# Performance work log

Hardware: AMD Instinct MI355X
Metric: run time of the kernel (lower is better)

## Reference

```python
import jax, jax.numpy as jnp
import numpy as np

N_NODES = 50000
N_EDGES = 800000
IN_CH = 64
OUT_CH = 64
HEADS = 4
NEG_SLOPE = 0.2  # PyG GATConv default


def setup_inputs() -> dict:
    key = jax.random.key(0)
    ks = jax.random.split(key, 8)
    x = jax.random.normal(ks[0], (N_NODES, IN_CH), dtype=jnp.float32)
    edge_index = jax.random.randint(ks[1], (2, N_EDGES), 0, N_NODES, dtype=jnp.int64)
    # GATConv params (concat=False): lin weight [in, H*out], att vectors [H, out], bias [out]
    W = jax.random.normal(ks[2], (IN_CH, HEADS * OUT_CH), dtype=jnp.float32) * (1.0 / np.sqrt(IN_CH))
    att_src = jax.random.normal(ks[3], (HEADS, OUT_CH), dtype=jnp.float32) * 0.1
    att_dst = jax.random.normal(ks[4], (HEADS, OUT_CH), dtype=jnp.float32) * 0.1
    bias = jnp.zeros((OUT_CH,), dtype=jnp.float32)
    fc_w = jax.random.normal(ks[5], (OUT_CH, 1), dtype=jnp.float32) * (1.0 / np.sqrt(OUT_CH))
    fc_b = jnp.zeros((1,), dtype=jnp.float32)
    return {"x": x, "edge_index": edge_index, "W": W, "att_src": att_src,
            "att_dst": att_dst, "bias": bias, "fc_w": fc_w, "fc_b": fc_b}


def reference(x, edge_index, W, att_src, att_dst, bias, fc_w, fc_b):
    N = x.shape[0]
    H, C = att_src.shape
    # per-node linear transform -> [N, H, C]
    xt = (x @ W).reshape(N, H, C)
    # PyG default add_self_loops=True
    loop = jnp.arange(N, dtype=edge_index.dtype)
    src = jnp.concatenate([edge_index[0], loop])  # message source j
    dst = jnp.concatenate([edge_index[1], loop])  # aggregation target i
    # attention logits: a_l . x_j + a_r . x_i, leaky_relu
    a_src = jnp.einsum('nhc,hc->nh', xt, att_src)  # [N, H]
    a_dst = jnp.einsum('nhc,hc->nh', xt, att_dst)
    e = jax.nn.leaky_relu(a_src[src] + a_dst[dst], NEG_SLOPE)  # [E, H]
    # segment softmax over incoming edges of each dst node
    m = jax.ops.segment_max(e, dst, num_segments=N)            # [N, H]
    e = jnp.exp(e - m[dst])
    s = jax.ops.segment_sum(e, dst, num_segments=N)            # [N, H]
    alpha = e / s[dst]                                          # [E, H]
    # weighted scatter-aggregate
    msg = xt[src] * alpha[:, :, None]                           # [E, H, C]
    out = jax.ops.segment_sum(msg, dst, num_segments=N)         # [N, H, C]
    out = out.mean(axis=1) + bias                               # concat=False -> mean heads
    h = jax.nn.relu(out)
    scores = (h @ fc_w + fc_b).squeeze(-1)                      # [N]
    return scores
```

## Files before the change

kernel.cpp:

```cpp
#include <hip/hip_runtime.h>
#include <hip/hip_bf16.h>

#define N_NODES 50000
#define N_EDGES 800000
#define HEADS   4
#define NEG_SLOPE 0.2f
#define CAP     64
#define NT      ((N_NODES + 63) / 64)
#define EPB     2048
#define NREG    391
#define NREP    8
#define QSUB    384
#define NAGG    (N_NODES / 16)
#define INV_LN2 1.44269504088896340736f

typedef __attribute__((ext_vector_type(8))) _Float16 half8;
typedef __attribute__((ext_vector_type(4))) float f32x4;
typedef __attribute__((ext_vector_type(8))) unsigned short u16x8;

template <typename T> __device__ __forceinline__ float cvt(T v);
template <> __device__ __forceinline__ float cvt<float>(float v) { return v; }
template <> __device__ __forceinline__ float cvt<__hip_bfloat16>(__hip_bfloat16 v) {
    return __bfloat162float(v);
}
__device__ __forceinline__ unsigned short f2h(float f) {
    _Float16 h = (_Float16)f;
    return __builtin_bit_cast(unsigned short, h);
}
__device__ __forceinline__ float hbits(unsigned short u) {
    return (float)__builtin_bit_cast(_Float16, u);
}
__device__ __forceinline__ int probe_fp32(const unsigned* xw) {
    int sane = 0;
    for (int j = 0; j < 64; ++j) {
        unsigned e = (xw[j] >> 7) & 0xFF;
        sane += (e >= 90 && e <= 141);
    }
    return sane < 32;
}
__device__ __forceinline__ float loadW(int isf32, const void* W, int idx) {
    return isf32 ? ((const float*)W)[idx]
                 : cvt<__hip_bfloat16>(((const __hip_bfloat16*)W)[idx]);
}

template <typename T>
__device__ __forceinline__ void load8_f16(const T* p, _Float16* dst);
template <>
__device__ __forceinline__ void load8_f16<float>(const float* p, _Float16* dst) {
    float4 a = *(const float4*)p;
    float4 b = *(const float4*)(p + 4);
    dst[0] = (_Float16)a.x; dst[1] = (_Float16)a.y;
    dst[2] = (_Float16)a.z; dst[3] = (_Float16)a.w;
    dst[4] = (_Float16)b.x; dst[5] = (_Float16)b.y;
    dst[6] = (_Float16)b.z; dst[7] = (_Float16)b.w;
}
template <>
__device__ __forceinline__ void load8_f16<__hip_bfloat16>(const __hip_bfloat16* p,
                                                          _Float16* dst) {
    uint4 a = *(const uint4*)p;
    const unsigned short* u = (const unsigned short*)&a;
#pragma unroll
    for (int j = 0; j < 8; ++j)
        dst[j] = (_Float16)__uint_as_float(((unsigned)u[j]) << 16);
}

__global__ __launch_bounds__(256) void k_init(const unsigned* __restrict__ xw,
                                              const int* __restrict__ ei,
                                              const void* __restrict__ W,
                                              const void* __restrict__ att_src,
                                              const void* __restrict__ att_dst,
                                              int* __restrict__ qcnt,
                                              int* __restrict__ flags,
                                              unsigned short* __restrict__ Batt,
                                              unsigned short* __restrict__ Bpost) {
    __shared__ float waS[256], waD[256];
    __shared__ int f32sh;
    if (blockIdx.x == 0) {
        for (int t = threadIdx.x; t < NREP * NREG; t += 256) qcnt[t] = 0;
        if (threadIdx.x == 0) {
            int all0 = 1;
            for (int j = 1; j < 64; j += 2) all0 &= (ei[j] == 0);
            flags[0] = all0;
            flags[1] = probe_fp32(xw);
        }
        return;
    }
    const int pb = blockIdx.x - 1;
    if (threadIdx.x == 0) f32sh = probe_fp32(xw);
    __syncthreads();
    const int isf32 = f32sh;
    if (pb == 0) {
        int t = threadIdx.x, k = t >> 2, h = t & 3;
        float s = 0.f, d = 0.f;
        for (int c = 0; c < 64; ++c) {
            float w = loadW(isf32, W, k * 256 + h * 64 + c);
            float as = isf32 ? ((const float*)att_src)[h * 64 + c]
                             : cvt<__hip_bfloat16>(((const __hip_bfloat16*)att_src)[h * 64 + c]);
            float ad = isf32 ? ((const float*)att_dst)[h * 64 + c]
                             : cvt<__hip_bfloat16>(((const __hip_bfloat16*)att_dst)[h * 64 + c]);
            s = fmaf(w, as, s);
            d = fmaf(w, ad, d);
        }
        waS[t] = s * INV_LN2;
        waD[t] = d * INV_LN2;
        __syncthreads();
        if (threadIdx.x < 128) {
            int r = threadIdx.x;
            int q = (r >> 6) & 1, l = r & 63, n = l & 15;
            int kbase = q * 32 + ((l >> 4) & 3) * 8;
#pragma unroll
            for (int j = 0; j < 8; ++j) {
                int kk = kbase + j;
                float v = (n < 4) ? waS[kk * 4 + n]
                        : (n < 8) ? waD[kk * 4 + (n - 4)] : 0.f;
                Batt[r * 8 + j] = f2h(v);
            }
        }
    } else {
        const int sub = threadIdx.x >> 5, s = threadIdx.x & 31;
        const int t = (pb - 1) * 8 + sub;
        const int kt = t >> 2, nt = t & 3;
#pragma unroll
        for (int e = 0; e < 16; ++e) {
            int idx = s * 16 + e;
            int l = idx >> 3, j = idx & 7;
            int rs = kt * 32 + ((l >> 4) & 3) * 8 + j;
            int h = rs >> 6, k_in = rs & 63;
            int c = nt * 16 + (l & 15);
            Bpost[t * 512 + l * 8 + j] =
                f2h(loadW(isf32, W, k_in * 256 + h * 64 + c) * 0.25f);
        }
    }
}

template <typename T>
__device__ __forceinline__ void row_body(const T* __restrict__ x,
                                         const unsigned short* __restrict__ Batt,
                                         unsigned short* __restrict__ x16,
                                         float* __restrict__ a_src,
                                         float* __restrict__ a_dst) {
    const int tid = threadIdx.x;
    const int wav = tid >> 6, lane = tid & 63;
    const int quad = lane >> 4, r15 = lane & 15;
    const int m0 = blockIdx.x * 64;
    const int grow_a = m0 + wav * 16 + r15;
    int gr = grow_a;
    if (gr >= N_NODES) gr = N_NODES - 1;
    half8 afrag[2];
#pragma unroll
    for (int q = 0; q < 2; ++q) {
        _Float16 tmp[8];
        load8_f16<T>(x + (size_t)gr * 64 + q * 32 + quad * 8, tmp);
#pragma unroll
        for (int j = 0; j < 8; ++j) afrag[q][j] = tmp[j];
    }
    if (grow_a < N_NODES) {
#pragma unroll
        for (int q = 0; q < 2; ++q)
            *(half8*)(x16 + (size_t)grow_a * 64 + q * 32 + quad * 8) = afrag[q];
    }
    f32x4 acc = (f32x4){0.f, 0.f, 0.f, 0.f};
    const half8* bp = (const half8*)Batt;
    acc = __builtin_amdgcn_mfma_f32_16x16x32_f16(afrag[0], bp[lane], acc, 0, 0, 0);
    acc = __builtin_amdgcn_mfma_f32_16x16x32_f16(afrag[1], bp[64 + lane], acc, 0, 0, 0);
    if (r15 < 8) {
#pragma unroll
        for (int r = 0; r < 4; ++r) {
            int grow = m0 + wav * 16 + quad * 4 + r;
            if (grow < N_NODES) {
                if (r15 < 4) a_src[grow * HEADS + r15]       = acc[r];
                else         a_dst[grow * HEADS + (r15 - 4)] = acc[r];
            }
        }
    }
}

__global__ __launch_bounds__(256) void k_mid(const void* __restrict__ x,
                                             const unsigned short* __restrict__ Batt,
                                             const int* __restrict__ ei,
                                             const int* __restrict__ flags,
                                             int* __restrict__ qcnt,
                                             unsigned* __restrict__ queue,
                                             unsigned short* __restrict__ x16,
                                             float* __restrict__ a_src,
                                             float* __restrict__ a_dst) {
    __shared__ int hist[NREG];
    __shared__ int qbaseS[NREG];
    const int tid = threadIdx.x;
    const bool edge_blk = ((blockIdx.x & 1) == 0);
    const int eb = blockIdx.x >> 1;
    const int rep = eb & (NREP - 1);
    unsigned rec[8]; int reg[8], lpos[8];
    int histv0 = 0, histv1 = 0, mybase0 = 0, mybase1 = 0;
    if (edge_blk) {
        for (int t = tid; t < NREG; t += 256) hist[t] = 0;
        __syncthreads();
        const int f64 = flags[0];
        const int pbase = eb * 1024 + tid;
#pragma unroll
        for (int k = 0; k < 4; ++k) {
            int pid = pbase + k * 256;
            int e = 2 * pid;
            if (e < N_EDGES) {
                int s0, d0, s1, d1;
                if (f64) {
                    int4 sv = *(const int4*)(ei + 2 * e);
                    int4 dv = *(const int4*)(ei + 2 * N_EDGES + 2 * e);
                    s0 = sv.x; s1 = sv.z; d0 = dv.x; d1 = dv.z;
                } else {
                    int2 sv = *(const int2*)(ei + e);
                    int2 dv = *(const int2*)(ei + N_EDGES + e);
                    s0 = sv.x; s1 = sv.y; d0 = dv.x; d1 = dv.y;
                }
                reg[2 * k]     = d0 >> 7;
                rec[2 * k]     = (unsigned)s0 | ((unsigned)d0 << 16);
                reg[2 * k + 1] = d1 >> 7;
                rec[2 * k + 1] = (unsigned)s1 | ((unsigned)d1 << 16);
            } else { reg[2 * k] = -1; reg[2 * k + 1] = -1; }
        }
#pragma unroll
        for (int k = 0; k < 8; ++k)
            if (reg[k] >= 0) lpos[k] = atomicAdd(&hist[reg[k]], 1);
        __syncthreads();
        {
            int t0 = tid, t1 = tid + 256;
            histv0 = hist[t0];
            if (histv0) mybase0 = atomicAdd(qcnt + rep * NREG + t0, histv0);
            if (t1 < NREG) {
                histv1 = hist[t1];
                if (histv1) mybase1 = atomicAdd(qcnt + rep * NREG + t1, histv1);
            }
        }
    }
    if (flags[1]) row_body<float>((const float*)x, Batt, x16, a_src, a_dst);
    else          row_body<__hip_bfloat16>((const __hip_bfloat16*)x, Batt,
                                           x16, a_src, a_dst);
    if (edge_blk) {
        qbaseS[tid] = mybase0;
        if (tid + 256 < NREG) qbaseS[tid + 256] = mybase1;
        __syncthreads();
#pragma unroll
        for (int k = 0; k < 8; ++k)
            if (reg[k] >= 0) {
                int o = qbaseS[reg[k]] + lpos[k];
                if (o < QSUB)
                    queue[((size_t)reg[k] * NREP + rep) * QSUB + o] = rec[k];
            }
    }
}

__global__ __launch_bounds__(256) void k_scat(const unsigned* __restrict__ queue,
                                              const int* __restrict__ qcnt,
                                              unsigned short* __restrict__ col_pad) {
    __shared__ int cl[128];
    __shared__ int mr[NREP];
    const int b = blockIdx.x, tid = threadIdx.x;
    const int base = b << 7;
    if (tid < 128) cl[tid] = 0;
    if (tid < NREP) {
        int m = qcnt[tid * NREG + b];
        mr[tid] = m > QSUB ? QSUB : m;
    }
    __syncthreads();
#pragma unroll
    for (int rep = 0; rep < NREP; ++rep) {
        int m = mr[rep];
        const unsigned* q = queue + ((size_t)b * NREP + rep) * QSUB;
        for (int i = tid; i < m; i += 256) {
            unsigned rec = q[i];
            int d = rec >> 16, s = rec & 0xffff;
            int p = atomicAdd(&cl[d - base], 1);
            if (p < CAP - 1) col_pad[(size_t)d * CAP + p] = (unsigned short)s;
        }
    }
    __syncthreads();
    if (tid < 128) {
        int j = base + tid;
        if (j < N_NODES) {
            int c = cl[tid]; c = c > CAP - 1 ? CAP - 1 : c;
            col_pad[(size_t)j * CAP + (CAP - 1)] = (unsigned short)c;
        }
    }
}

template <typename T>
__device__ __forceinline__ void agg_body(const unsigned short* __restrict__ col_pad,
                                         const float* __restrict__ a_src,
                                         const float* __restrict__ a_dst,
                                         const unsigned short* __restrict__ x16,
                                         const unsigned short* __restrict__ Bpost,
                                         const T* __restrict__ bias,
                                         const T* __restrict__ fc_w,
                                         const T* __restrict__ fc_b,
                                         float* __restrict__ out,
                                         int* __restrict__ cS,
                                         float4* __restrict__ peS,
                                         unsigned* __restrict__ sS,
                                         float* __restrict__ postS) {
    const int tid = threadIdx.x;
    const int wav = tid >> 6, lane = tid & 63;
    const int hlf = lane >> 5, l5 = lane & 31;
    const int quad = lane >> 4, r15 = lane & 15;
    const int nbase = blockIdx.x * 16 + wav * 4;
    int* cSw = cS + wav * 64;
    float4* peSw = peS + wav * 64;
    const int slot = (lane & 1) * 32 + (lane >> 1);
    const char* xb = (const char*)x16 + l5 * 4;
    int cval = (int)col_pad[(size_t)nbase * CAP + lane];
#pragma unroll
    for (int nid = 0; nid < 4; ++nid) {
        const int wid = nbase + nid;
        int cval_next = 0;
        if (nid < 3)
            cval_next = (int)col_pad[(size_t)(wid + 1) * CAP + lane];
        const int n = __shfl(cval, 63, 64);
        const float4 ad = ((const float4*)a_dst)[wid];
        const int mycol = (lane < n) ? cval : wid;
        const float4 as = ((const float4*)a_src)[mycol];
        float e0 = as.x + ad.x, e1 = as.y + ad.y;
        float e2 = as.z + ad.z, e3 = as.w + ad.w;
        e0 = e0 > 0.f ? e0 : NEG_SLOPE * e0;  e1 = e1 > 0.f ? e1 : NEG_SLOPE * e1;
        e2 = e2 > 0.f ? e2 : NEG_SLOPE * e2;  e3 = e3 > 0.f ? e3 : NEG_SLOPE * e3;
        float4 pe = make_float4(exp2f(e0), exp2f(e1), exp2f(e2), exp2f(e3));
        if (lane > n) pe = make_float4(0.f, 0.f, 0.f, 0.f);
        cSw[slot] = mycol << 7;
        peSw[slot] = pe;
        float a0 = 0.f, a1 = 0.f, a2 = 0.f, a3 = 0.f;
        float a4 = 0.f, a5 = 0.f, a6 = 0.f, a7 = 0.f;
        float sp0 = 0.f, sp1 = 0.f, sp2 = 0.f, sp3 = 0.f;
        const int nr = (n + 2) >> 1;
        const int*    cB = cSw + hlf * 32;
        const float4* pB = peSw + hlf * 32;
#define ACC2(D, P) { float x0 = hbits((unsigned short)((D) & 0xffff)); \
                     float x1 = hbits((unsigned short)((D) >> 16)); \
                     a0 = fmaf((P).x, x0, a0); a1 = fmaf((P).x, x1, a1); \
                     a2 = fmaf((P).y, x0, a2); a3 = fmaf((P).y, x1, a3); \
                     a4 = fmaf((P).z, x0, a4); a5 = fmaf((P).z, x1, a5); \
                     a6 = fmaf((P).w, x0, a6); a7 = fmaf((P).w, x1, a7); \
                     sp0 += (P).x; sp1 += (P).y; sp2 += (P).z; sp3 += (P).w; }
        int r = 0;
        for (; r + 8 <= nr; r += 8) {
            const int4 cc0 = *(const int4*)(cB + r);
            const int4 cc1 = *(const int4*)(cB + r + 4);
            unsigned dA = *(const unsigned*)(xb + cc0.x);
            unsigned dB = *(const unsigned*)(xb + cc0.y);
            unsigned dC = *(const unsigned*)(xb + cc0.z);
            unsigned dD = *(const unsigned*)(xb + cc0.w);
            unsigned dE = *(const unsigned*)(xb + cc1.x);
            unsigned dF = *(const unsigned*)(xb + cc1.y);
            unsigned dG = *(const unsigned*)(xb + cc1.z);
            unsigned dH = *(const unsigned*)(xb + cc1.w);
            float4 pA = pB[r],     pBv = pB[r + 1];
            float4 pC = pB[r + 2], pD  = pB[r + 3];
            float4 pE = pB[r + 4], pF  = pB[r + 5];
            float4 pG = pB[r + 6], pH  = pB[r + 7];
            ACC2(dA, pA); ACC2(dB, pBv); ACC2(dC, pC); ACC2(dD, pD);
            ACC2(dE, pE); ACC2(dF, pF);  ACC2(dG, pG); ACC2(dH, pH);
        }
        for (; r + 4 <= nr; r += 4) {
            const int4 cc = *(const int4*)(cB + r);
            unsigned dA = *(const unsigned*)(xb + cc.x);
            unsigned dB = *(const unsigned*)(xb + cc.y);
            unsigned dC = *(const unsigned*)(xb + cc.z);
            unsigned dD = *(const unsigned*)(xb + cc.w);
            float4 pA = pB[r], pBv = pB[r + 1], pC = pB[r + 2], pD = pB[r + 3];
            ACC2(dA, pA); ACC2(dB, pBv); ACC2(dC, pC); ACC2(dD, pD);
        }
        for (; r < nr; ++r) {
            int c = cB[r];
            unsigned d = *(const unsigned*)(xb + c);
            float4 p = pB[r];
            ACC2(d, p);
        }
#undef ACC2
        a0 += __shfl_xor(a0, 32, 64); a1 += __shfl_xor(a1, 32, 64);
        a2 += __shfl_xor(a2, 32, 64); a3 += __shfl_xor(a3, 32, 64);
        a4 += __shfl_xor(a4, 32, 64); a5 += __shfl_xor(a5, 32, 64);
        a6 += __shfl_xor(a6, 32, 64); a7 += __shfl_xor(a7, 32, 64);
        sp0 += __shfl_xor(sp0, 32, 64); sp1 += __shfl_xor(sp1, 32, 64);
        sp2 += __shfl_xor(sp2, 32, 64); sp3 += __shfl_xor(sp3, 32, 64);
        const float r0 = 1.f / sp0, r1 = 1.f / sp1;
        const float r2 = 1.f / sp2, r3 = 1.f / sp3;
        if (lane < 32) {
            unsigned* sr = sS + (wav * 4 + nid) * 132;
            sr[l5]      = (unsigned)f2h(a0 * r0) | ((unsigned)f2h(a1 * r0) << 16);
            sr[32 + l5] = (unsigned)f2h(a2 * r1) | ((unsigned)f2h(a3 * r1) << 16);
            sr[64 + l5] = (unsigned)f2h(a4 * r2) | ((unsigned)f2h(a5 * r2) << 16);
            sr[96 + l5] = (unsigned)f2h(a6 * r3) | ((unsigned)f2h(a7 * r3) << 16);
        }
        cval = cval_next;
    }
    __syncthreads();
    {
        const int nt = wav;
        f32x4 acc = (f32x4){0.f, 0.f, 0.f, 0.f};
        const half8* bp = (const half8*)Bpost;
#pragma unroll
        for (int kt = 0; kt < 8; ++kt) {
            half8 af = *(const half8*)&sS[r15 * 132 + kt * 16 + quad * 4];
            acc = __builtin_amdgcn_mfma_f32_16x16x32_f16(
                af, bp[(kt * 4 + nt) * 64 + lane], acc, 0, 0, 0);
        }
        const float bi = cvt<T>(bias[nt * 16 + r15]);
        const float fw = cvt<T>(fc_w[nt * 16 + r15]);
#pragma unroll
        for (int rr = 0; rr < 4; ++rr) {
            float o = acc[rr] + bi;
            o = o > 0.f ? o : 0.f;
            float p = o * fw;
            p += __shfl_xor(p, 1, 64); p += __shfl_xor(p, 2, 64);
            p += __shfl_xor(p, 4, 64); p += __shfl_xor(p, 8, 64);
            if (r15 == 0) postS[(quad * 4 + rr) * 4 + nt] = p;
        }
    }
    __syncthreads();
    if (tid < 16) {
        float o = postS[tid * 4] + postS[tid * 4 + 1]
                + postS[tid * 4 + 2] + postS[tid * 4 + 3] + cvt<T>(fc_b[0]);
        out[blockIdx.x * 16 + tid] = o;
    }
}

__global__ __launch_bounds__(256) void k_aggregate(
        const unsigned short* __restrict__ col_pad,
        const float* __restrict__ a_src,
        const float* __restrict__ a_dst,
        const unsigned short* __restrict__ x16,
        const unsigned short* __restrict__ Bpost,
        const void* __restrict__ bias,
        const void* __restrict__ fc_w,
        const void* __restrict__ fc_b,
        const int* __restrict__ flags,
        float* __restrict__ out) {
    __shared__ __align__(16) int cS[4 * 64];
    __shared__ float4 peS[4 * 64];
    __shared__ __align__(16) unsigned sS[16 * 132];
    __shared__ float postS[16 * 4];
    if (flags[1])
        agg_body<float>(col_pad, a_src, a_dst, x16, Bpost, (const float*)bias,
                        (const float*)fc_w, (const float*)fc_b, out,
                        cS, peS, sS, postS);
    else
        agg_body<__hip_bfloat16>(col_pad, a_src, a_dst, x16, Bpost,
                                 (const __hip_bfloat16*)bias,
                                 (const __hip_bfloat16*)fc_w,
                                 (const __hip_bfloat16*)fc_b, out,
                                 cS, peS, sS, postS);
}

extern "C" void kernel_launch(void* const* d_in, const int* in_sizes, int n_in,
                              void* d_out, int out_size, void* d_ws, size_t ws_size,
                              hipStream_t stream) {
    const void* x       = d_in[0];
    const int*  ei      = (const int*)d_in[1];
    const void* W       = d_in[2];
    const void* att_src = d_in[3];
    const void* att_dst = d_in[4];
    const void* bias    = d_in[5];
    const void* fc_w    = d_in[6];
    const void* fc_b    = d_in[7];
    float* out = (float*)d_out;

    char* wsb = (char*)d_ws;
    unsigned short* x16   = (unsigned short*)wsb;
    unsigned*       queue = (unsigned*)(wsb + 6400000);
    unsigned short* col_pad = (unsigned short*)(wsb + 11204608);
    float* a_src = (float*)(wsb + 17604608);
    float* a_dst = (float*)(wsb + 18404608);
    unsigned short* Batt  = (unsigned short*)(wsb + 19204608);
    unsigned short* Bpost = (unsigned short*)(wsb + 19206656);
    int* flags = (int*)(wsb + 19239424);
    int* qcnt  = (int*)(wsb + 19239432);

    k_init<<<6, 256, 0, stream>>>((const unsigned*)x, ei, W, att_src,
                                  att_dst, qcnt, flags, Batt, Bpost);
    k_mid<<<NT, 256, 0, stream>>>(x, Batt, ei, flags, qcnt, queue,
                                  x16, a_src, a_dst);
    k_scat<<<NREG, 256, 0, stream>>>(queue, qcnt, col_pad);
    k_aggregate<<<NAGG, 256, 0, stream>>>(col_pad, a_src, a_dst, x16, Bpost,
                                          bias, fc_w, fc_b, flags, out);
}
```

Measured before the change: 156.2 us.

## Halve edge-binning blocks and move softmax denominator to wave butterfly reduction

The fused mid kernel now makes only every fourth block an edge-binning block, with each handling twice as many edges (16 per thread), and EPB is doubled to match. The region index is recomputed from the packed record instead of being stored, which saves registers. In the aggregation kernel the softmax denominator is computed once with a full-wave xor butterfly over the per-edge exponentials, replacing the per-iteration adds in the gather loop. This trades fewer global atomics and a lighter inner loop for more serial work per binning block and extra shuffles.

```diff
diff --git a/kernel.cpp b/kernel.cpp
--- a/kernel.cpp
+++ b/kernel.cpp
@@ -7,7 +7,7 @@
 #define NEG_SLOPE 0.2f
 #define CAP     64
 #define NT      ((N_NODES + 63) / 64)
-#define EPB     2048
+#define EPB     4096
 #define NREG    391
 #define NREP    8
 #define QSUB    384
@@ -187,18 +187,18 @@
     __shared__ int hist[NREG];
     __shared__ int qbaseS[NREG];
     const int tid = threadIdx.x;
-    const bool edge_blk = ((blockIdx.x & 1) == 0);
-    const int eb = blockIdx.x >> 1;
+    const bool edge_blk = ((blockIdx.x & 3) == 0);
+    const int eb = blockIdx.x >> 2;
     const int rep = eb & (NREP - 1);
-    unsigned rec[8]; int reg[8], lpos[8];
+    unsigned rec[16]; int lpos[16];
     int histv0 = 0, histv1 = 0, mybase0 = 0, mybase1 = 0;
     if (edge_blk) {
         for (int t = tid; t < NREG; t += 256) hist[t] = 0;
         __syncthreads();
         const int f64 = flags[0];
-        const int pbase = eb * 1024 + tid;
-#pragma unroll
-        for (int k = 0; k < 4; ++k) {
+        const int pbase = eb * 2048 + tid;
+#pragma unroll
+        for (int k = 0; k < 8; ++k) {
             int pid = pbase + k * 256;
             int e = 2 * pid;
             if (e < N_EDGES) {
@@ -212,15 +212,14 @@
                     int2 dv = *(const int2*)(ei + N_EDGES + e);
                     s0 = sv.x; s1 = sv.y; d0 = dv.x; d1 = dv.y;
                 }
-                reg[2 * k]     = d0 >> 7;
                 rec[2 * k]     = (unsigned)s0 | ((unsigned)d0 << 16);
-                reg[2 * k + 1] = d1 >> 7;
                 rec[2 * k + 1] = (unsigned)s1 | ((unsigned)d1 << 16);
-            } else { reg[2 * k] = -1; reg[2 * k + 1] = -1; }
-        }
-#pragma unroll
-        for (int k = 0; k < 8; ++k)
-            if (reg[k] >= 0) lpos[k] = atomicAdd(&hist[reg[k]], 1);
+                lpos[2 * k] = 0; lpos[2 * k + 1] = 0;
+            } else { lpos[2 * k] = -1; lpos[2 * k + 1] = -1; }
+        }
+#pragma unroll
+        for (int k = 0; k < 16; ++k)
+            if (lpos[k] >= 0) lpos[k] = atomicAdd(&hist[rec[k] >> 23], 1);
         __syncthreads();
         {
             int t0 = tid, t1 = tid + 256;
@@ -240,11 +239,12 @@
         if (tid + 256 < NREG) qbaseS[tid + 256] = mybase1;
         __syncthreads();
 #pragma unroll
-        for (int k = 0; k < 8; ++k)
-            if (reg[k] >= 0) {
-                int o = qbaseS[reg[k]] + lpos[k];
+        for (int k = 0; k < 16; ++k)
+            if (lpos[k] >= 0) {
+                int reg = rec[k] >> 23;
+                int o = qbaseS[reg] + lpos[k];
                 if (o < QSUB)
-                    queue[((size_t)reg[k] * NREP + rep) * QSUB + o] = rec[k];
+                    queue[((size_t)reg * NREP + rep) * QSUB + o] = rec[k];
             }
     }
 }
@@ -325,9 +325,16 @@
         if (lane > n) pe = make_float4(0.f, 0.f, 0.f, 0.f);
         cSw[slot] = mycol << 7;
         peSw[slot] = pe;
+        float sp0 = pe.x, sp1 = pe.y, sp2 = pe.z, sp3 = pe.w;
+#pragma unroll
+        for (int off = 1; off < 64; off <<= 1) {
+            sp0 += __shfl_xor(sp0, off, 64);
+            sp1 += __shfl_xor(sp1, off, 64);
+            sp2 += __shfl_xor(sp2, off, 64);
+            sp3 += __shfl_xor(sp3, off, 64);
+        }
         float a0 = 0.f, a1 = 0.f, a2 = 0.f, a3 = 0.f;
         float a4 = 0.f, a5 = 0.f, a6 = 0.f, a7 = 0.f;
-        float sp0 = 0.f, sp1 = 0.f, sp2 = 0.f, sp3 = 0.f;
         const int nr = (n + 2) >> 1;
         const int*    cB = cSw + hlf * 32;
         const float4* pB = peSw + hlf * 32;
@@ -336,8 +343,7 @@
                      a0 = fmaf((P).x, x0, a0); a1 = fmaf((P).x, x1, a1); \
                      a2 = fmaf((P).y, x0, a2); a3 = fmaf((P).y, x1, a3); \
                      a4 = fmaf((P).z, x0, a4); a5 = fmaf((P).z, x1, a5); \
-                     a6 = fmaf((P).w, x0, a6); a7 = fmaf((P).w, x1, a7); \
-                     sp0 += (P).x; sp1 += (P).y; sp2 += (P).z; sp3 += (P).w; }
+                     a6 = fmaf((P).w, x0, a6); a7 = fmaf((P).w, x1, a7); }
         int r = 0;
         for (; r + 8 <= nr; r += 8) {
             const int4 cc0 = *(const int4*)(cB + r);
@@ -377,8 +383,6 @@
         a2 += __shfl_xor(a2, 32, 64); a3 += __shfl_xor(a3, 32, 64);
         a4 += __shfl_xor(a4, 32, 64); a5 += __shfl_xor(a5, 32, 64);
         a6 += __shfl_xor(a6, 32, 64); a7 += __shfl_xor(a7, 32, 64);
-        sp0 += __shfl_xor(sp0, 32, 64); sp1 += __shfl_xor(sp1, 32, 64);
-        sp2 += __shfl_xor(sp2, 32, 64); sp3 += __shfl_xor(sp3, 32, 64);
         const float r0 = 1.f / sp0, r1 = 1.f / sp1;
         const float r2 = 1.f / sp2, r3 = 1.f / sp3;
         if (lane < 32) {
```

Result: slower. 169.2 us (+8.3%).
